# Performance work log

Hardware: AMD Instinct MI355X
Metric: run time of the kernel (lower is better)

Reference implementation:

```python
import jax, jax.numpy as jnp
import numpy as np

D_MODEL = 1024
N_HEADS = 16
D_K = D_MODEL // N_HEADS
B, S = 2, 2048


def setup_inputs() -> dict:
    key = jax.random.key(0)
    ks = jax.random.split(key, 11)
    s = 1.0 / np.sqrt(D_MODEL)
    return {
        "q": jax.random.normal(ks[0], (B, S, D_MODEL), jnp.float32),
        "k": jax.random.normal(ks[1], (B, S, D_MODEL), jnp.float32),
        "v": jax.random.normal(ks[2], (B, S, D_MODEL), jnp.float32),
        "Wq": jax.random.normal(ks[3], (D_MODEL, D_MODEL), jnp.float32) * s,
        "bq": jnp.zeros((D_MODEL,), jnp.float32),
        "Wk": jax.random.normal(ks[4], (D_MODEL, D_MODEL), jnp.float32) * s,
        "bk": jnp.zeros((D_MODEL,), jnp.float32),
        "Wv": jax.random.normal(ks[5], (D_MODEL, D_MODEL), jnp.float32) * s,
        "bv": jnp.zeros((D_MODEL,), jnp.float32),
        "Wo": jax.random.normal(ks[6], (D_MODEL, D_MODEL), jnp.float32) * s,
        "bo": jnp.zeros((D_MODEL,), jnp.float32),
    }


def reference(q, k, v, Wq, bq, Wk, bk, Wv, bv, Wo, bo):
    b = q.shape[0]
    # linear projections then split heads: [b, s, d] -> [b, h, s, d_k]
    def proj(x, W, bias):
        y = jnp.einsum('bsd,ed->bse', x, W) + bias  # torch Linear: x @ W.T + b
        return y.reshape(b, -1, N_HEADS, D_K).transpose(0, 2, 1, 3)

    qh, kh, vh = proj(q, Wq, bq), proj(k, Wk, bk), proj(v, Wv, bv)
    scores = jnp.einsum('bhqd,bhkd->bhqk', qh, kh) / np.sqrt(D_K)
    attn = jax.nn.softmax(scores, axis=-1)  # dropout: identity (eval mode)
    x = jnp.einsum('bhqk,bhkd->bhqd', attn, vh)
    x = x.transpose(0, 2, 1, 3).reshape(b, -1, D_MODEL)
    return jnp.einsum('bsd,ed->bse', x, Wo) + bo
```

## Files before the change

kernel.cpp:

```cpp
#include <hip/hip_runtime.h>
#include <math.h>
#include <stdint.h>

#define DM 1024
#define NH 16
#define DKH 64
#define BB 2
#define SS 2048
#define MM (BB*SS)

typedef __bf16 bf16;
typedef __bf16 bf16x8 __attribute__((ext_vector_type(8)));
typedef __bf16 bf16x4 __attribute__((ext_vector_type(4)));
typedef short s16x4 __attribute__((ext_vector_type(4)));
typedef float f32x4 __attribute__((ext_vector_type(4)));

#define MFMA16(a,b,c) __builtin_amdgcn_mfma_f32_16x16x32_bf16((a),(b),(c),0,0,0)

#if __has_builtin(__builtin_amdgcn_mfma_f32_16x16x16bf16_1k)
#define MFMAK16(a,b,c) __builtin_amdgcn_mfma_f32_16x16x16bf16_1k((a),(b),(c),0,0,0)
#else
__device__ static inline f32x4 mfma_k16_asm(s16x4 a, s16x4 b, f32x4 c) {
  asm("v_mfma_f32_16x16x16_bf16 %0, %1, %2, %0" : "+v"(c) : "v"(a), "v"(b));
  return c;
}
#define MFMAK16(a,b,c) mfma_k16_asm((a),(b),(c))
#endif

#define QSCALE 0.1803368801111204f

__device__ static inline void g2l16(const void* g, void* l) {
  __builtin_amdgcn_global_load_lds(
      (const __attribute__((address_space(1))) unsigned int*)g,
      (__attribute__((address_space(3))) unsigned int*)l, 16, 0, 0);
}

__global__ __launch_bounds__(256) void cvt_all(
    const float* __restrict__ q, const float* __restrict__ k, const float* __restrict__ v,
    const float* __restrict__ wq, const float* __restrict__ wk,
    const float* __restrict__ wv, const float* __restrict__ wo,
    bf16* __restrict__ Xq, bf16* __restrict__ Xk, bf16* __restrict__ Xv,
    bf16* __restrict__ Wqb, bf16* __restrict__ Wkb, bf16* __restrict__ Wvb,
    bf16* __restrict__ Wob)
{
  const long i = (long)blockIdx.x * 256 + threadIdx.x;
  const float* src; bf16* dst; long off;
  if (i < 3L * 524288L) {
    const int a = (int)(i / 524288L);
    off = (i % 524288L) * 8;
    src = (a == 0) ? q : (a == 1) ? k : v;
    dst = (a == 0) ? Xq : (a == 1) ? Xk : Xv;
  } else {
    const long j = i - 3L * 524288L;
    const int a = (int)(j / 131072L);
    off = (j % 131072L) * 8;
    src = (a == 0) ? wq : (a == 1) ? wk : (a == 2) ? wv : wo;
    dst = (a == 0) ? Wqb : (a == 1) ? Wkb : (a == 2) ? Wvb : Wob;
  }
  float4 f0 = *(const float4*)(src + off);
  float4 f1 = *(const float4*)(src + off + 4);
  bf16x8 o;
  o[0] = (bf16)f0.x; o[1] = (bf16)f0.y; o[2] = (bf16)f0.z; o[3] = (bf16)f0.w;
  o[4] = (bf16)f1.x; o[5] = (bf16)f1.y; o[6] = (bf16)f1.z; o[7] = (bf16)f1.w;
  *(bf16x8*)(dst + off) = o;
}

template<int EP, int BN>
__device__ __forceinline__ void gemm_bt_body(
    const bf16* __restrict__ A, const bf16* __restrict__ W,
    const float* __restrict__ bias, void* __restrict__ Y, float scale)
{
  constexpr int NT = BN / 32;
  constexpr int PB = BN / 32;
  __shared__ __align__(16) char smem[16384 + BN * 128];
  const int tid = threadIdx.x;
  const int lane = tid & 63, w = tid >> 6;
  const int ln15 = lane & 15, q4 = lane >> 4;
  const int m0 = blockIdx.x * 128;
  const int n0 = blockIdx.y * BN;
  const int mhalf = (w >> 1) * 64, nhalf = (w & 1) * (BN / 2);

  const bf16* gA[4]; const bf16* gB[PB];
  char* lA[4]; char* lB[PB];
  #pragma unroll
  for (int p = 0; p < 4; ++p) {
    const int n = p * 256 + tid;
    const int row = n >> 3, u = n & 7;
    const int g = u ^ (row & 7);
    gA[p] = A + (size_t)(m0 + row) * DM + g * 8;
    lA[p] = smem + n * 16;
  }
  #pragma unroll
  for (int p = 0; p < PB; ++p) {
    const int n = p * 256 + tid;
    const int row = n >> 3, u = n & 7;
    const int g = u ^ (row & 7);
    gB[p] = W + (size_t)(n0 + row) * DM + g * 8;
    lB[p] = smem + 16384 + n * 16;
  }

  int aoff[4][2], boff[NT][2];
  #pragma unroll
  for (int mt = 0; mt < 4; ++mt) {
    const int row = mhalf + mt * 16 + ln15;
    #pragma unroll
    for (int kc = 0; kc < 2; ++kc)
      aoff[mt][kc] = (row * 8 + ((kc * 4 + q4) ^ (row & 7))) * 16;
  }
  #pragma unroll
  for (int nt = 0; nt < NT; ++nt) {
    const int row = nhalf + nt * 16 + ln15;
    #pragma unroll
    for (int kc = 0; kc < 2; ++kc)
      boff[nt][kc] = 16384 + (row * 8 + ((kc * 4 + q4) ^ (row & 7))) * 16;
  }

  f32x4 acc[4][NT] = {};

  for (int kt = 0; kt < DM; kt += 64) {
    __syncthreads();
    #pragma unroll
    for (int p = 0; p < 4; ++p) g2l16(gA[p] + kt, lA[p]);
    #pragma unroll
    for (int p = 0; p < PB; ++p) g2l16(gB[p] + kt, lB[p]);
    asm volatile("s_waitcnt vmcnt(0)" ::: "memory");
    __syncthreads();
    #pragma unroll
    for (int kc = 0; kc < 2; ++kc) {
      bf16x8 af[4];
      #pragma unroll
      for (int mt = 0; mt < 4; ++mt) af[mt] = *(const bf16x8*)(smem + aoff[mt][kc]);
      #pragma unroll
      for (int nt = 0; nt < NT; ++nt) {
        bf16x8 bfr = *(const bf16x8*)(smem + boff[nt][kc]);
        #pragma unroll
        for (int mt = 0; mt < 4; ++mt)
          acc[mt][nt] = MFMA16(af[mt], bfr, acc[mt][nt]);
      }
    }
  }

  #pragma unroll
  for (int nt = 0; nt < NT; ++nt) {
    const int col = n0 + nhalf + nt * 16 + ln15;
    const float bv = bias[col];
    #pragma unroll
    for (int mt = 0; mt < 4; ++mt) {
      #pragma unroll
      for (int r = 0; r < 4; ++r) {
        const int row = m0 + mhalf + mt * 16 + q4 * 4 + r;
        const float val = (acc[mt][nt][r] + bv) * scale;
        if (EP == 0) {
          ((float*)Y)[(size_t)row * DM + col] = val;
        } else {
          const int b = row >> 11, s = row & 2047;
          const int h = col >> 6, dk = col & 63;
          ((bf16*)Y)[(((size_t)(b * NH + h) * SS + s) * DKH) + dk] = (bf16)val;
        }
      }
    }
  }
}

__global__ __launch_bounds__(256) void gemm_qkv(
    const bf16* Xq, const bf16* Xk, const bf16* Xv,
    const bf16* Wq, const bf16* Wk, const bf16* Wv,
    const float* bq, const float* bk, const float* bv,
    bf16* qh, bf16* kh, bf16* vh)
{
  const int z = blockIdx.z;
  const bf16* A = (z == 0) ? Xq : (z == 1) ? Xk : Xv;
  const bf16* W = (z == 0) ? Wq : (z == 1) ? Wk : Wv;
  const float* bias = (z == 0) ? bq : (z == 1) ? bk : bv;
  bf16* Y = (z == 0) ? qh : (z == 1) ? kh : vh;
  const float scale = (z == 0) ? QSCALE : 1.0f;
  gemm_bt_body<1, 128>(A, W, bias, Y, scale);
}

__global__ __launch_bounds__(256) void gemm_out(
    const bf16* A, const bf16* W, const float* bias, float* Y)
{
  gemm_bt_body<0, 64>(A, W, bias, Y, 1.0f);
}

__global__ __launch_bounds__(256) void transpose_v(
    const bf16* __restrict__ vh, bf16* __restrict__ vth)
{
  __shared__ unsigned short Ls[64][66];
  const int bh = blockIdx.y;
  const int s0 = blockIdx.x * 64;
  const int tid = threadIdx.x;
  const unsigned short* src = (const unsigned short*)(vh + (size_t)bh * SS * DKH);
  unsigned short* dst = (unsigned short*)(vth + (size_t)bh * SS * DKH);
  #pragma unroll
  for (int p = 0; p < 2; ++p) {
    const int n = p * 256 + tid;
    const int sl = n >> 3, dc = (n & 7) * 8;
    uint4 a = *(const uint4*)(src + (size_t)(s0 + sl) * DKH + dc);
    Ls[sl][dc + 0] = (unsigned short)(a.x & 0xffff);
    Ls[sl][dc + 1] = (unsigned short)(a.x >> 16);
    Ls[sl][dc + 2] = (unsigned short)(a.y & 0xffff);
    Ls[sl][dc + 3] = (unsigned short)(a.y >> 16);
    Ls[sl][dc + 4] = (unsigned short)(a.z & 0xffff);
    Ls[sl][dc + 5] = (unsigned short)(a.z >> 16);
    Ls[sl][dc + 6] = (unsigned short)(a.w & 0xffff);
    Ls[sl][dc + 7] = (unsigned short)(a.w >> 16);
  }
  __syncthreads();
  #pragma unroll
  for (int p = 0; p < 2; ++p) {
    const int n = p * 256 + tid;
    const int dk = n >> 3, sc = (n & 7) * 8;
    uint4 o;
    o.x = (unsigned)Ls[sc + 0][dk] | ((unsigned)Ls[sc + 1][dk] << 16);
    o.y = (unsigned)Ls[sc + 2][dk] | ((unsigned)Ls[sc + 3][dk] << 16);
    o.z = (unsigned)Ls[sc + 4][dk] | ((unsigned)Ls[sc + 5][dk] << 16);
    o.w = (unsigned)Ls[sc + 6][dk] | ((unsigned)Ls[sc + 7][dk] << 16);
    if (dk & 8) { uint4 t = o; o.x = t.z; o.y = t.w; o.z = t.x; o.w = t.y; }
    *(uint4*)(dst + (size_t)dk * SS + s0 + sc) = o;
  }
}

template<int CUR, int VM, bool PF>
__device__ __forceinline__ void attn_slot(
    char* smem, const bf16*& gKc, const bf16*& gVc, const int st0,
    const int (&koff)[2][2], const int (&voff)[2][4],
    const bf16x8 (&qf)[4][2], const s16x4 onesf, const f32x4 Zf,
    f32x4 (&Oa)[4][4], f32x4 (&Ol)[4])
{
  if constexpr (VM == 4) asm volatile("s_waitcnt vmcnt(4)" ::: "memory");
  else                   asm volatile("s_waitcnt vmcnt(0)" ::: "memory");
  __builtin_amdgcn_s_barrier();
  asm volatile("" ::: "memory");
  if constexpr (PF) {
    constexpr int NB = (CUR + 2) & 3;
    char* d = smem + NB * 16384 + st0;
    g2l16(gKc,          d);
    g2l16(gKc + 2048,   d + 4096);
    g2l16(gVc,          d + 8192);
    g2l16(gVc + 65536,  d + 12288);
    gKc += 4096; gVc += 64;
  }
  bf16x8 kf[2][2];
  #pragma unroll
  for (int nt = 0; nt < 2; ++nt)
    #pragma unroll
    for (int kc = 0; kc < 2; ++kc)
      kf[nt][kc] = *(const bf16x8*)(smem + CUR * 16384 + koff[nt][kc]);
  s16x4 vf[2][4];
  #pragma unroll
  for (int nt = 0; nt < 2; ++nt)
    #pragma unroll
    for (int dt = 0; dt < 4; ++dt)
      vf[nt][dt] = *(const s16x4*)(smem + CUR * 16384 + voff[nt][dt]);

  f32x4 S[2][4];
  #pragma unroll
  for (int nt = 0; nt < 2; ++nt)
    #pragma unroll
    for (int mt = 0; mt < 4; ++mt) {
      S[nt][mt] = MFMA16(kf[nt][0], qf[mt][0], Zf);
      S[nt][mt] = MFMA16(kf[nt][1], qf[mt][1], S[nt][mt]);
    }

  #pragma unroll
  for (int nt = 0; nt < 2; ++nt)
    #pragma unroll
    for (int mt = 0; mt < 4; ++mt) {
      const float p0 = __builtin_amdgcn_exp2f(S[nt][mt][0]);
      const float p1 = __builtin_amdgcn_exp2f(S[nt][mt][1]);
      const float p2 = __builtin_amdgcn_exp2f(S[nt][mt][2]);
      const float p3 = __builtin_amdgcn_exp2f(S[nt][mt][3]);
      union { bf16x4 b; s16x4 s; } u;
      u.b[0] = (bf16)p0; u.b[1] = (bf16)p1; u.b[2] = (bf16)p2; u.b[3] = (bf16)p3;
      const s16x4 pf = u.s;
      #pragma unroll
      for (int dt = 0; dt < 4; ++dt)
        Oa[mt][dt] = MFMAK16(pf, vf[nt][dt], Oa[mt][dt]);
      Ol[mt] = MFMAK16(pf, onesf, Ol[mt]);
    }
}

__global__ __launch_bounds__(256, 2) void attn_mfma(
    const bf16* __restrict__ Qh, const bf16* __restrict__ Kh,
    const bf16* __restrict__ Vth, bf16* __restrict__ Xout)
{
  __shared__ __align__(16) char smem[65536];
  const int tid = threadIdx.x, lane = tid & 63, w = tid >> 6;
  const int ln15 = lane & 15, q4 = lane >> 4;
  const int bh = blockIdx.x, b = bh >> 4, h = bh & 15;
  const int qh = w >> 1, kh = w & 1;
  const int q0 = blockIdx.y * 128 + qh * 64;
  const bf16* Qb = Qh + (size_t)bh * SS * DKH;
  const bf16* Kb = Kh + (size_t)bh * SS * DKH;
  const bf16* Vb = Vth + (size_t)bh * SS * DKH;

  bf16x8 qf[4][2];
  #pragma unroll
  for (int mt = 0; mt < 4; ++mt)
    #pragma unroll
    for (int kc = 0; kc < 2; ++kc)
      qf[mt][kc] = *(const bf16x8*)(Qb + (size_t)(q0 + mt * 16 + ln15) * DKH + kc * 32 + q4 * 8);
  asm volatile("s_waitcnt vmcnt(0)" ::: "memory");

  int koff[2][2], voff[2][4];
  #pragma unroll
  for (int nt = 0; nt < 2; ++nt) {
    const int row = kh * 32 + nt * 16 + ln15;
    #pragma unroll
    for (int kc = 0; kc < 2; ++kc)
      koff[nt][kc] = (row * 8 + ((kc * 4 + q4) ^ (row & 7))) * 16;
    #pragma unroll
    for (int dt = 0; dt < 4; ++dt) {
      const int vr = dt * 16 + ln15;
      const int u = kh * 4 + nt * 2 + (q4 >> 1);
      voff[nt][dt] = 8192 + (vr * 8 + (u ^ (vr & 7))) * 16
                   + ((q4 ^ (ln15 >> 3)) & 1) * 8;
    }
  }

  s16x4 onesf;
  {
    const bf16 o1 = (ln15 == 0) ? (bf16)1.0f : (bf16)0.0f;
    union { bf16x4 b; s16x4 s; } u;
    u.b[0] = o1; u.b[1] = o1; u.b[2] = o1; u.b[3] = o1;
    onesf = u.s;
  }
  const f32x4 Zf = {0.f, 0.f, 0.f, 0.f};

  const int rowS = tid >> 3, uS = tid & 7;
  const int gS = uS ^ (rowS & 7);
  const bf16* gKc = Kb + (size_t)rowS * DKH + gS * 8;
  const bf16* gVc = Vb + (size_t)rowS * SS + gS * 8;
  const int st0 = tid * 16;

  f32x4 Oa[4][4] = {};
  f32x4 Ol[4] = {};

  {
    char* d0 = smem + st0;
    g2l16(gKc, d0); g2l16(gKc + 2048, d0 + 4096);
    g2l16(gVc, d0 + 8192); g2l16(gVc + 65536, d0 + 12288);
    gKc += 4096; gVc += 64;
    char* d1 = smem + 16384 + st0;
    g2l16(gKc, d1); g2l16(gKc + 2048, d1 + 4096);
    g2l16(gVc, d1 + 8192); g2l16(gVc + 65536, d1 + 12288);
    gKc += 4096; gVc += 64;
  }

  #pragma unroll 1
  for (int it = 0; it < 7; ++it) {
    attn_slot<0, 4, true >(smem, gKc, gVc, st0, koff, voff, qf, onesf, Zf, Oa, Ol);
    attn_slot<1, 4, true >(smem, gKc, gVc, st0, koff, voff, qf, onesf, Zf, Oa, Ol);
    attn_slot<2, 4, true >(smem, gKc, gVc, st0, koff, voff, qf, onesf, Zf, Oa, Ol);
    attn_slot<3, 4, true >(smem, gKc, gVc, st0, koff, voff, qf, onesf, Zf, Oa, Ol);
  }
  attn_slot<0, 4, true >(smem, gKc, gVc, st0, koff, voff, qf, onesf, Zf, Oa, Ol);
  attn_slot<1, 4, true >(smem, gKc, gVc, st0, koff, voff, qf, onesf, Zf, Oa, Ol);
  attn_slot<2, 4, false>(smem, gKc, gVc, st0, koff, voff, qf, onesf, Zf, Oa, Ol);
  attn_slot<3, 0, false>(smem, gKc, gVc, st0, koff, voff, qf, onesf, Zf, Oa, Ol);

  __syncthreads();
  if (w & 1) {
    char* R = smem + (w >> 1) * 16384;
    #pragma unroll
    for (int mt = 0; mt < 4; ++mt)
      #pragma unroll
      for (int dt = 0; dt < 4; ++dt)
        *(f32x4*)(R + ((mt * 4 + dt) * 64 + lane) * 16) = Oa[mt][dt];
    char* Rl = smem + 32768 + (w >> 1) * 4096;
    #pragma unroll
    for (int mt = 0; mt < 4; ++mt)
      *(f32x4*)(Rl + (mt * 64 + lane) * 16) = Ol[mt];
  }
  __syncthreads();
  if (!(w & 1)) {
    char* R = smem + (w >> 1) * 16384;
    #pragma unroll
    for (int mt = 0; mt < 4; ++mt)
      #pragma unroll
      for (int dt = 0; dt < 4; ++dt)
        Oa[mt][dt] += *(const f32x4*)(R + ((mt * 4 + dt) * 64 + lane) * 16);
    char* Rl = smem + 32768 + (w >> 1) * 4096;
    #pragma unroll
    for (int mt = 0; mt < 4; ++mt)
      Ol[mt] += *(const f32x4*)(Rl + (mt * 64 + lane) * 16);

    #pragma unroll
    for (int mt = 0; mt < 4; ++mt)
      #pragma unroll
      for (int r = 0; r < 4; ++r) {
        const float l = __shfl(Ol[mt][r], lane & 48);
        const float inv = 1.f / l;
        const int srow = q0 + mt * 16 + q4 * 4 + r;
        #pragma unroll
        for (int dt = 0; dt < 4; ++dt) {
          const int col = h * DKH + dt * 16 + ln15;
          Xout[((size_t)(b * SS + srow)) * DM + col] = (bf16)(Oa[mt][dt][r] * inv);
        }
      }
  }
}

extern "C" void kernel_launch(void* const* d_in, const int* in_sizes, int n_in,
                              void* d_out, int out_size, void* d_ws, size_t ws_size,
                              hipStream_t stream)
{
  const float* q  = (const float*)d_in[0];
  const float* k  = (const float*)d_in[1];
  const float* v  = (const float*)d_in[2];
  const float* Wq = (const float*)d_in[3];
  const float* bq = (const float*)d_in[4];
  const float* Wk = (const float*)d_in[5];
  const float* bk = (const float*)d_in[6];
  const float* Wv = (const float*)d_in[7];
  const float* bv = (const float*)d_in[8];
  const float* Wo = (const float*)d_in[9];
  const float* bo = (const float*)d_in[10];
  float* out = (float*)d_out;

  char* ws = (char*)d_ws;
  const size_t MB = 1u << 20;
  bf16* Xq  = (bf16*)(ws + 0);
  bf16* Xk  = (bf16*)(ws + 8 * MB);
  bf16* Xv  = (bf16*)(ws + 16 * MB);
  bf16* Wqb = (bf16*)(ws + 24 * MB);
  bf16* Wkb = (bf16*)(ws + 26 * MB);
  bf16* Wvb = (bf16*)(ws + 28 * MB);
  bf16* Wob = (bf16*)(ws + 30 * MB);
  bf16* qh  = (bf16*)(ws + 32 * MB);
  bf16* kh  = (bf16*)(ws + 40 * MB);
  bf16* vh  = (bf16*)(ws + 48 * MB);
  bf16* vth = (bf16*)(ws + 56 * MB);
  bf16* xh  = Xq;

  cvt_all<<<8192, 256, 0, stream>>>(q, k, v, Wq, Wk, Wv, Wo,
                                    Xq, Xk, Xv, Wqb, Wkb, Wvb, Wob);

  gemm_qkv<<<dim3(32, 8, 3), 256, 0, stream>>>(Xq, Xk, Xv, Wqb, Wkb, Wvb,
                                               bq, bk, bv, qh, kh, vh);

  transpose_v<<<dim3(32, 32), 256, 0, stream>>>(vh, vth);

  attn_mfma<<<dim3(32, 16), 256, 0, stream>>>(qh, kh, vth, xh);

  gemm_out<<<dim3(32, 16), 256, 0, stream>>>(xh, Wob, bo, out);
}
```

Before: 216.4 us.

## Halve attention query tile, use double buffering, raise occupancy and MFMA priority

The attention kernel now processes 64 queries per block instead of 128, which doubles the grid to 1024 blocks. Shared memory drops from a 4-stage to a 2-stage K/V ring (32 KB), and launch bounds request 4 blocks per CU. MFMA sections are wrapped in s_setprio so waves doing matrix math get issue priority. The aim is more waves per CU to hide latency and keep tensor cores busy, at the cost of reloading each K/V tile for twice as many blocks and a shallower prefetch depth (waitcnt now goes to zero every slot).

```diff
diff --git a/kernel.cpp b/kernel.cpp
--- a/kernel.cpp
+++ b/kernel.cpp
@@ -221,20 +221,18 @@
   }
 }
 
-template<int CUR, int VM, bool PF>
+template<int CUR, bool PF>
 __device__ __forceinline__ void attn_slot(
     char* smem, const bf16*& gKc, const bf16*& gVc, const int st0,
     const int (&koff)[2][2], const int (&voff)[2][4],
-    const bf16x8 (&qf)[4][2], const s16x4 onesf, const f32x4 Zf,
-    f32x4 (&Oa)[4][4], f32x4 (&Ol)[4])
-{
-  if constexpr (VM == 4) asm volatile("s_waitcnt vmcnt(4)" ::: "memory");
-  else                   asm volatile("s_waitcnt vmcnt(0)" ::: "memory");
+    const bf16x8 (&qf)[2][2], const s16x4 onesf, const f32x4 Zf,
+    f32x4 (&Oa)[2][4], f32x4 (&Ol)[2])
+{
+  asm volatile("s_waitcnt vmcnt(0)" ::: "memory");
   __builtin_amdgcn_s_barrier();
   asm volatile("" ::: "memory");
   if constexpr (PF) {
-    constexpr int NB = (CUR + 2) & 3;
-    char* d = smem + NB * 16384 + st0;
+    char* d = smem + (CUR ^ 1) * 16384 + st0;
     g2l16(gKc,          d);
     g2l16(gKc + 2048,   d + 4096);
     g2l16(gVc,          d + 8192);
@@ -254,11 +252,12 @@
     for (int dt = 0; dt < 4; ++dt)
       vf[nt][dt] = *(const s16x4*)(smem + CUR * 16384 + voff[nt][dt]);
 
-  f32x4 S[2][4];
+  __builtin_amdgcn_s_setprio(1);
+  f32x4 S[2][2];
   #pragma unroll
   for (int nt = 0; nt < 2; ++nt)
     #pragma unroll
-    for (int mt = 0; mt < 4; ++mt) {
+    for (int mt = 0; mt < 2; ++mt) {
       S[nt][mt] = MFMA16(kf[nt][0], qf[mt][0], Zf);
       S[nt][mt] = MFMA16(kf[nt][1], qf[mt][1], S[nt][mt]);
     }
@@ -266,7 +265,7 @@
   #pragma unroll
   for (int nt = 0; nt < 2; ++nt)
     #pragma unroll
-    for (int mt = 0; mt < 4; ++mt) {
+    for (int mt = 0; mt < 2; ++mt) {
       const float p0 = __builtin_amdgcn_exp2f(S[nt][mt][0]);
       const float p1 = __builtin_amdgcn_exp2f(S[nt][mt][1]);
       const float p2 = __builtin_amdgcn_exp2f(S[nt][mt][2]);
@@ -279,25 +278,26 @@
         Oa[mt][dt] = MFMAK16(pf, vf[nt][dt], Oa[mt][dt]);
       Ol[mt] = MFMAK16(pf, onesf, Ol[mt]);
     }
-}
-
-__global__ __launch_bounds__(256, 2) void attn_mfma(
+  __builtin_amdgcn_s_setprio(0);
+}
+
+__global__ __launch_bounds__(256, 4) void attn_mfma(
     const bf16* __restrict__ Qh, const bf16* __restrict__ Kh,
     const bf16* __restrict__ Vth, bf16* __restrict__ Xout)
 {
-  __shared__ __align__(16) char smem[65536];
+  __shared__ __align__(16) char smem[32768];
   const int tid = threadIdx.x, lane = tid & 63, w = tid >> 6;
   const int ln15 = lane & 15, q4 = lane >> 4;
   const int bh = blockIdx.x, b = bh >> 4, h = bh & 15;
   const int qh = w >> 1, kh = w & 1;
-  const int q0 = blockIdx.y * 128 + qh * 64;
+  const int q0 = blockIdx.y * 64 + qh * 32;
   const bf16* Qb = Qh + (size_t)bh * SS * DKH;
   const bf16* Kb = Kh + (size_t)bh * SS * DKH;
   const bf16* Vb = Vth + (size_t)bh * SS * DKH;
 
-  bf16x8 qf[4][2];
-  #pragma unroll
-  for (int mt = 0; mt < 4; ++mt)
+  bf16x8 qf[2][2];
+  #pragma unroll
+  for (int mt = 0; mt < 2; ++mt)
     #pragma unroll
     for (int kc = 0; kc < 2; ++kc)
       qf[mt][kc] = *(const bf16x8*)(Qb + (size_t)(q0 + mt * 16 + ln15) * DKH + kc * 32 + q4 * 8);
@@ -334,60 +334,52 @@
   const bf16* gVc = Vb + (size_t)rowS * SS + gS * 8;
   const int st0 = tid * 16;
 
-  f32x4 Oa[4][4] = {};
-  f32x4 Ol[4] = {};
+  f32x4 Oa[2][4] = {};
+  f32x4 Ol[2] = {};
 
   {
     char* d0 = smem + st0;
     g2l16(gKc, d0); g2l16(gKc + 2048, d0 + 4096);
     g2l16(gVc, d0 + 8192); g2l16(gVc + 65536, d0 + 12288);
     gKc += 4096; gVc += 64;
-    char* d1 = smem + 16384 + st0;
-    g2l16(gKc, d1); g2l16(gKc + 2048, d1 + 4096);
-    g2l16(gVc, d1 + 8192); g2l16(gVc + 65536, d1 + 12288);
-    gKc += 4096; gVc += 64;
   }
 
   #pragma unroll 1
-  for (int it = 0; it < 7; ++it) {
-    attn_slot<0, 4, true >(smem, gKc, gVc, st0, koff, voff, qf, onesf, Zf, Oa, Ol);
-    attn_slot<1, 4, true >(smem, gKc, gVc, st0, koff, voff, qf, onesf, Zf, Oa, Ol);
-    attn_slot<2, 4, true >(smem, gKc, gVc, st0, koff, voff, qf, onesf, Zf, Oa, Ol);
-    attn_slot<3, 4, true >(smem, gKc, gVc, st0, koff, voff, qf, onesf, Zf, Oa, Ol);
-  }
-  attn_slot<0, 4, true >(smem, gKc, gVc, st0, koff, voff, qf, onesf, Zf, Oa, Ol);
-  attn_slot<1, 4, true >(smem, gKc, gVc, st0, koff, voff, qf, onesf, Zf, Oa, Ol);
-  attn_slot<2, 4, false>(smem, gKc, gVc, st0, koff, voff, qf, onesf, Zf, Oa, Ol);
-  attn_slot<3, 0, false>(smem, gKc, gVc, st0, koff, voff, qf, onesf, Zf, Oa, Ol);
+  for (int it = 0; it < 15; ++it) {
+    attn_slot<0, true >(smem, gKc, gVc, st0, koff, voff, qf, onesf, Zf, Oa, Ol);
+    attn_slot<1, true >(smem, gKc, gVc, st0, koff, voff, qf, onesf, Zf, Oa, Ol);
+  }
+  attn_slot<0, true >(smem, gKc, gVc, st0, koff, voff, qf, onesf, Zf, Oa, Ol);
+  attn_slot<1, false>(smem, gKc, gVc, st0, koff, voff, qf, onesf, Zf, Oa, Ol);
 
   __syncthreads();
-  if (w & 1) {
-    char* R = smem + (w >> 1) * 16384;
-    #pragma unroll
-    for (int mt = 0; mt < 4; ++mt)
+  if (kh) {
+    char* R = smem + qh * 8192;
+    #pragma unroll
+    for (int mt = 0; mt < 2; ++mt)
       #pragma unroll
       for (int dt = 0; dt < 4; ++dt)
         *(f32x4*)(R + ((mt * 4 + dt) * 64 + lane) * 16) = Oa[mt][dt];
-    char* Rl = smem + 32768 + (w >> 1) * 4096;
-    #pragma unroll
-    for (int mt = 0; mt < 4; ++mt)
+    char* Rl = smem + 16384 + qh * 2048;
+    #pragma unroll
+    for (int mt = 0; mt < 2; ++mt)
       *(f32x4*)(Rl + (mt * 64 + lane) * 16) = Ol[mt];
   }
   __syncthreads();
-  if (!(w & 1)) {
-    char* R = smem + (w >> 1) * 16384;
-    #pragma unroll
-    for (int mt = 0; mt < 4; ++mt)
+  if (!kh) {
+    char* R = smem + qh * 8192;
+    #pragma unroll
+    for (int mt = 0; mt < 2; ++mt)
       #pragma unroll
       for (int dt = 0; dt < 4; ++dt)
         Oa[mt][dt] += *(const f32x4*)(R + ((mt * 4 + dt) * 64 + lane) * 16);
-    char* Rl = smem + 32768 + (w >> 1) * 4096;
-    #pragma unroll
-    for (int mt = 0; mt < 4; ++mt)
+    char* Rl = smem + 16384 + qh * 2048;
+    #pragma unroll
+    for (int mt = 0; mt < 2; ++mt)
       Ol[mt] += *(const f32x4*)(Rl + (mt * 64 + lane) * 16);
 
     #pragma unroll
-    for (int mt = 0; mt < 4; ++mt)
+    for (int mt = 0; mt < 2; ++mt)
       #pragma unroll
       for (int r = 0; r < 4; ++r) {
         const float l = __shfl(Ol[mt][r], lane & 48);
@@ -442,7 +434,7 @@
 
   transpose_v<<<dim3(32, 32), 256, 0, stream>>>(vh, vth);
 
-  attn_mfma<<<dim3(32, 16), 256, 0, stream>>>(qh, kh, vth, xh);
+  attn_mfma<<<dim3(32, 32), 256, 0, stream>>>(qh, kh, vth, xh);
 
   gemm_out<<<dim3(32, 16), 256, 0, stream>>>(xh, Wob, bo, out);
 }
```

After: 212.5 us. Within noise of the previous version (-1.8%).
